# Optimization experiments

Hardware: AMD Instinct MI355X
Metric: run time of the kernel (lower is better)

## Reference

```python
import jax, jax.numpy as jnp
import numpy as np

K = 3          # deform conv kernel size
PAD = 1        # (K-1)//2
DG = 4         # deformable groups
C_IN = 256     # sum(in_channel_list)
C_OUT = 256


def setup_inputs() -> dict:
    key = jax.random.key(0)
    k0, k1, k2, k3, k4, k5 = jax.random.split(key, 6)
    B, H, W = 2, 64, 256
    x0 = jax.random.normal(k0, (B, 64, H, W), dtype=jnp.float32)
    x1 = jax.random.normal(k1, (B, 64, H, W), dtype=jnp.float32)
    x2 = jax.random.normal(k2, (B, 128, H, W), dtype=jnp.float32)
    # conv_offset: 1x1 conv, weight zero-inited in the module; we use small
    # random weights so offsets are spatially varying (nontrivial sampling).
    w_off = jax.random.normal(k3, (DG * K * K * 2, C_IN), dtype=jnp.float32) * 0.01
    b_off = jax.random.normal(k4, (DG * K * K * 2,), dtype=jnp.float32) * 0.5
    # deform conv weight [O, C, K*K] (flat kernel, row-major i*K+j), no bias (mmcv DeformConv)
    w_def = jax.random.normal(k5, (C_OUT, C_IN, K * K), dtype=jnp.float32) / np.sqrt(C_IN * K * K)
    return {"x0": x0, "x1": x1, "x2": x2, "w_off": w_off, "b_off": b_off, "w_def": w_def}


def _deform_gather(xg, py, px):
    # xg: [B, DG, Cg, H, W] grouped input; py/px: [B, DG, K2, H, W] abs sample coords
    B, dg, Cg, H, W = xg.shape
    K2 = py.shape[2]
    y0f = jnp.floor(py)
    x0f = jnp.floor(px)
    wy = py - y0f  # fractional parts
    wx = px - x0f
    y0 = y0f.astype(jnp.int32)
    x0 = x0f.astype(jnp.int32)
    xf = xg.reshape(B, dg, Cg, H * W)

    def corner(yi, xi, w):
        valid = ((yi >= 0) & (yi <= H - 1) & (xi >= 0) & (xi <= W - 1)).astype(xg.dtype)
        idx = jnp.clip(yi, 0, H - 1) * W + jnp.clip(xi, 0, W - 1)   # [B,dg,K2,H,W]
        idxf = idx.reshape(B, dg, 1, K2 * H * W)
        g = jnp.take_along_axis(xf, jnp.broadcast_to(idxf, (B, dg, Cg, K2 * H * W)), axis=-1)
        g = g.reshape(B, dg, Cg, K2, H, W)
        return g * (w * valid)[:, :, None]  # broadcast over Cg

    return (corner(y0, x0, (1.0 - wy) * (1.0 - wx))
            + corner(y0, x0 + 1, (1.0 - wy) * wx)
            + corner(y0 + 1, x0, wy * (1.0 - wx))
            + corner(y0 + 1, x0 + 1, wy * wx))  # [B,dg,Cg,K2,H,W]


def reference(x0, x1, x2, w_off, b_off, w_def):
    x = jnp.concatenate([x0, x1, x2], axis=1)  # [B, C, H, W]
    B, C, H, W = x.shape
    # 1x1 offset conv
    off = jnp.einsum('bchw,oc->bohw', x, w_off) + b_off[None, :, None, None]
    off = off.reshape(B, DG, K * K, 2, H, W)
    dy = off[:, :, :, 0]  # [B,DG,K2,H,W]
    dx = off[:, :, :, 1]
    ky, kx = jnp.meshgrid(jnp.arange(K), jnp.arange(K), indexing='ij')
    ky = ky.reshape(-1).astype(jnp.float32)
    kx = kx.reshape(-1).astype(jnp.float32)
    hh = jnp.arange(H, dtype=jnp.float32)
    ww = jnp.arange(W, dtype=jnp.float32)
    py = hh[None, None, None, :, None] - PAD + ky[None, None, :, None, None] + dy
    px = ww[None, None, None, None, :] - PAD + kx[None, None, :, None, None] + dx
    xg = x.reshape(B, DG, C // DG, H, W)
    samp = _deform_gather(xg, py, px).reshape(B, C, K * K, H, W)
    out = jnp.einsum('bckhw,ock->bohw', samp, w_def)
    return jax.nn.relu(out)
```

## Files before the change

kernel.cpp:

```cpp
#include <hip/hip_runtime.h>


constexpr int H_ = 64, W_ = 256;
constexpr int HWsz = H_ * W_;
constexpr int OC_ = 256;
constexpr int WMAIN_ELEMS = 72 * 16 * 64 * 8;
constexpr int WOFFB_ELEMS = 8 * 5 * 64 * 8;
constexpr size_t XT_ELEMS = (size_t)8 * HWsz * 64;

using f32x4 = __attribute__((ext_vector_type(4))) float;
using s16x8 = __attribute__((ext_vector_type(8))) short;
using u16x8 = __attribute__((ext_vector_type(8))) unsigned short;
using u16x4 = __attribute__((ext_vector_type(4))) unsigned short;

__device__ __forceinline__ unsigned short f2bf(float f) {
    unsigned u = __float_as_uint(f);
    return (unsigned short)((u + 0x7fffu + ((u >> 16) & 1u)) >> 16);
}
__device__ __forceinline__ float bf2f(unsigned short u) {
    return __uint_as_float((unsigned)u << 16);
}
__device__ __forceinline__ void gload_lds16(const void* g, void* l) {
    __builtin_amdgcn_global_load_lds(
        (const __attribute__((address_space(1))) void*)g,
        (__attribute__((address_space(3))) void*)l, 16, 0, 0);
}


__global__ __launch_bounds__(256) void wprep_kernel(const float* __restrict__ w_def,
                                                    const float* __restrict__ w_off,
                                                    unsigned short* __restrict__ w2) {
    int i = blockIdx.x * 256 + threadIdx.x;
    if (i < WMAIN_ELEMS) {
        int j = i & 7, lane = (i >> 3) & 63, t = (i >> 9) & 15, gkh = i >> 13;
        int half = gkh & 1, gk = gkh >> 1;
        int k = gk % 9, g = gk / 9;
        int oc = t * 16 + (lane & 15);
        int cin = g * 64 + half * 32 + (lane >> 4) * 8 + j;
        w2[i] = f2bf(w_def[(size_t)oc * 2304 + (size_t)cin * 9 + k]);
    } else if (i < WMAIN_ELEMS + WOFFB_ELEMS) {
        int i2 = i - WMAIN_ELEMS;
        int j = i2 & 7, lane = (i2 >> 3) & 63, idx = i2 >> 9;
        int t = idx % 5, c8 = idx / 5;
        int o = t * 16 + (lane & 15);
        int ch = c8 * 32 + (lane >> 4) * 8 + j;
        float v = (o < 72) ? w_off[o * 256 + ch] : 0.f;
        w2[i] = f2bf(v);
    }
}

__global__ __launch_bounds__(256) void xprep_kernel(const float* __restrict__ x0,
                                                    const float* __restrict__ x1,
                                                    const float* __restrict__ x2,
                                                    unsigned short* __restrict__ xt) {
    __shared__ unsigned short tl[256][66];
    const int bg = blockIdx.x >> 6;
    const int y  = blockIdx.x & 63;
    const int b  = bg >> 2, g = bg & 3;
    const int tid = threadIdx.x;
    const float* src = (g == 0) ? x0 + (size_t)b * 64 * HWsz
                     : (g == 1) ? x1 + (size_t)b * 64 * HWsz
                     : x2 + (size_t)b * 128 * HWsz + (size_t)(g - 2) * 64 * HWsz;
    src += y * W_;
    for (int c = 0; c < 64; ++c)
        tl[tid][c] = f2bf(src[(size_t)c * HWsz + tid]);
    __syncthreads();
    unsigned short* dst = xt + ((size_t)bg * HWsz + y * W_) * 64;
    #pragma unroll
    for (int s = 0; s < 8; ++s) {
        int si = s * 256 + tid;
        int px = si >> 3, q = si & 7;
        u16x8 v;
        #pragma unroll
        for (int j = 0; j < 8; ++j) v[j] = tl[px][q * 8 + j];
        *(u16x8*)(dst + (size_t)px * 64 + q * 8) = v;
    }
}


struct GPre {
    float w00, w01, w10, w11;
    u16x4 c00, c01, c10, c11;
};

__global__ __launch_bounds__(512, 4) void deform64_kernel(
    const unsigned short* __restrict__ xt, const float* __restrict__ b_off,
    const unsigned short* __restrict__ w2, float* __restrict__ out)
{
    __shared__ float off_lds[72 * 64];
    __shared__ __align__(16) unsigned short Bbuf[2][8192];
    __shared__ __align__(16) unsigned short sbuf[2][2560];

    const int tid  = threadIdx.x;
    const int lane = tid & 63;
    const int wv   = tid >> 6;
    const int bid  = ((blockIdx.x & 7) << 6) | (blockIdx.x >> 3);
    const int xt4  = bid & 3;
    const int h    = (bid >> 2) & 63;
    const int b    = bid >> 8;
    const int xbase = xt4 * 64;
    const int nh   = wv & 1;
    const int pg   = wv >> 1;
    const int p16  = lane & 15;
    const int cq   = lane >> 4;
    const int bp   = wv * 8 + (lane >> 3);
    const int chg  = lane & 7;

    const unsigned short* xtb = xt + (size_t)b * 4 * HWsz * 64;

    if (wv < 4) {
        f32x4 oa[5];
        #pragma unroll
        for (int t = 0; t < 5; ++t) {
            int o = t * 16 + p16;
            float bv = (o < 72) ? b_off[o] : 0.f;
            oa[t][0] = bv; oa[t][1] = bv; oa[t][2] = bv; oa[t][3] = bv;
        }
        const int pixg = h * W_ + xbase + wv * 16;
        #pragma unroll
        for (int c8 = 0; c8 < 8; ++c8) {
            const unsigned short* ap = xtb + (size_t)(c8 >> 1) * HWsz * 64
                                     + (size_t)(pixg + p16) * 64 + (c8 & 1) * 32 + cq * 8;
            s16x8 a = *(const s16x8*)ap;
            const unsigned short* wb = w2 + WMAIN_ELEMS + (size_t)(c8 * 5) * 512;
            #pragma unroll
            for (int t = 0; t < 5; ++t) {
                s16x8 bf = *(const s16x8*)(wb + t * 512 + lane * 8);
                oa[t] = __builtin_amdgcn_mfma_f32_16x16x32_bf16(a, bf, oa[t], 0, 0, 0);
            }
        }
        #pragma unroll
        for (int t = 0; t < 5; ++t) {
            int o = t * 16 + p16;
            if (o < 72) {
                #pragma unroll
                for (int r = 0; r < 4; ++r)
                    off_lds[o * 64 + wv * 16 + cq * 4 + r] = oa[t][r];
            }
        }
    }
    __syncthreads();

    auto stageB = [&](int gkh, int bsel) {
        const char* src = (const char*)w2 + (size_t)gkh * 16384 + (size_t)tid * 16;
        char* dst = (char*)&Bbuf[bsel][0] + wv * 1024;
        gload_lds16(src, dst);
        gload_lds16(src + 8192, dst + 8192);
    };
    auto gpre = [&](int gkh) -> GPre {
        const int half = gkh & 1, gk = gkh >> 1;
        const int k = gk % 9, g = gk / 9;
        const int ky = k / 3, kx = k % 3;
        float dy = off_lds[(2 * gk) * 64 + bp];
        float dx = off_lds[(2 * gk + 1) * 64 + bp];
        float fy = (float)(h - 1 + ky) + dy;
        float fx = (float)(xbase + bp - 1 + kx) + dx;
        float y0f = floorf(fy), x0f = floorf(fx);
        float wy = fy - y0f, wx = fx - x0f;
        int iy0 = (int)y0f, ix0 = (int)x0f;
        int iy1 = iy0 + 1, ix1 = ix0 + 1;
        float vy0 = (iy0 >= 0 && iy0 < H_) ? 1.f : 0.f;
        float vy1 = (iy1 >= 0 && iy1 < H_) ? 1.f : 0.f;
        float vx0 = (ix0 >= 0 && ix0 < W_) ? 1.f : 0.f;
        float vx1 = (ix1 >= 0 && ix1 < W_) ? 1.f : 0.f;
        GPre G;
        G.w00 = (1.f - wy) * (1.f - wx) * vy0 * vx0;
        G.w01 = (1.f - wy) * wx * vy0 * vx1;
        G.w10 = wy * (1.f - wx) * vy1 * vx0;
        G.w11 = wy * wx * vy1 * vx1;
        int cy0 = min(max(iy0, 0), H_ - 1), cy1 = min(max(iy1, 0), H_ - 1);
        int cx0 = min(max(ix0, 0), W_ - 1), cx1 = min(max(ix1, 0), W_ - 1);
        const int eb = half * 32 + chg * 4;
        const unsigned short* src = xtb + (size_t)g * HWsz * 64;
        G.c00 = *(const u16x4*)(src + (cy0 * W_ + cx0) * 64 + eb);
        G.c01 = *(const u16x4*)(src + (cy0 * W_ + cx1) * 64 + eb);
        G.c10 = *(const u16x4*)(src + (cy1 * W_ + cx0) * 64 + eb);
        G.c11 = *(const u16x4*)(src + (cy1 * W_ + cx1) * 64 + eb);
        return G;
    };
    auto gpost = [&](const GPre& G, int bsel) {
        u16x4 res;
        #pragma unroll
        for (int j = 0; j < 4; ++j) {
            float v = fmaf(G.w00, bf2f(G.c00[j]), fmaf(G.w01, bf2f(G.c01[j]),
                      fmaf(G.w10, bf2f(G.c10[j]), G.w11 * bf2f(G.c11[j]))));
            res[j] = f2bf(v);
        }
        *(u16x4*)&sbuf[bsel][bp * 40 + chg * 4] = res;
    };

    f32x4 acc[8];
    #pragma unroll
    for (int t = 0; t < 8; ++t) { acc[t][0]=0; acc[t][1]=0; acc[t][2]=0; acc[t][3]=0; }

    stageB(0, 0);
    {
        GPre G0 = gpre(0);
        gpost(G0, 0);
    }
    __syncthreads();

    const int arow = (pg * 16 + p16) * 40 + cq * 8;
    const unsigned short* bbase0 = &Bbuf[0][0] + (nh * 8) * 512 + lane * 8;
    const unsigned short* bbase1 = &Bbuf[1][0] + (nh * 8) * 512 + lane * 8;

    for (int i = 0; i < 72; ++i) {
        const int cur = i & 1;
        GPre G;
        const bool pf = (i < 71);
        if (pf) {
            stageB(i + 1, cur ^ 1);
            G = gpre(i + 1);
        }
        __builtin_amdgcn_sched_barrier(0);
        s16x8 a = *(const s16x8*)&sbuf[cur][arow];
        const unsigned short* bb = cur ? bbase1 : bbase0;
        #pragma unroll
        for (int t = 0; t < 8; ++t) {
            s16x8 bf = *(const s16x8*)(bb + t * 512);
            acc[t] = __builtin_amdgcn_mfma_f32_16x16x32_bf16(a, bf, acc[t], 0, 0, 0);
        }
        __builtin_amdgcn_sched_barrier(0);
        if (pf) gpost(G, cur ^ 1);
        __syncthreads();
    }

    const size_t obase = (size_t)b * OC_ * HWsz + (size_t)h * W_
                       + xbase + pg * 16 + cq * 4;
    #pragma unroll
    for (int t = 0; t < 8; ++t) {
        int oc = nh * 128 + t * 16 + p16;
        float4 r;
        r.x = fmaxf(acc[t][0], 0.f);
        r.y = fmaxf(acc[t][1], 0.f);
        r.z = fmaxf(acc[t][2], 0.f);
        r.w = fmaxf(acc[t][3], 0.f);
        *(float4*)(out + obase + (size_t)oc * HWsz) = r;
    }
}


struct Geom {
    float w00, w01, w10, w11;
    int o00, o01, o10, o11;
    const float* base;
};

__device__ __forceinline__ Geom make_geom(
    int gkh, const float* offp, int h, int wbase, int p, int cq,
    const float* xA, const float* xB, const float* xC)
{
    const int half = gkh & 1, gk = gkh >> 1;
    const int k = gk % 9, g = gk / 9;
    const int ky = k / 3, kx = k % 3;
    float dy = offp[(2 * gk) * 16 + p];
    float dx = offp[(2 * gk + 1) * 16 + p];
    float fy = (float)(h - 1 + ky) + dy;
    float fx = (float)(wbase + p - 1 + kx) + dx;
    float y0f = floorf(fy), x0f = floorf(fx);
    float wy = fy - y0f, wx = fx - x0f;
    int iy0 = (int)y0f, ix0 = (int)x0f;
    int iy1 = iy0 + 1, ix1 = ix0 + 1;
    float vy0 = (iy0 >= 0 && iy0 < H_) ? 1.f : 0.f;
    float vy1 = (iy1 >= 0 && iy1 < H_) ? 1.f : 0.f;
    float vx0 = (ix0 >= 0 && ix0 < W_) ? 1.f : 0.f;
    float vx1 = (ix1 >= 0 && ix1 < W_) ? 1.f : 0.f;
    Geom gm;
    gm.w00 = (1.f - wy) * (1.f - wx) * vy0 * vx0;
    gm.w01 = (1.f - wy) * wx * vy0 * vx1;
    gm.w10 = wy * (1.f - wx) * vy1 * vx0;
    gm.w11 = wy * wx * vy1 * vx1;
    int cy0 = min(max(iy0, 0), H_ - 1), cy1 = min(max(iy1, 0), H_ - 1);
    int cx0 = min(max(ix0, 0), W_ - 1), cx1 = min(max(ix1, 0), W_ - 1);
    int choff = (half * 32 + cq * 8) * HWsz;
    gm.o00 = choff + cy0 * W_ + cx0;
    gm.o01 = choff + cy0 * W_ + cx1;
    gm.o10 = choff + cy1 * W_ + cx0;
    gm.o11 = choff + cy1 * W_ + cx1;
    gm.base = (g == 0) ? xA : (g == 1) ? xB : (g == 2) ? xC : xC + (size_t)64 * HWsz;
    return gm;
}

#define GATHER(J, Cv) do { \
    Cv.x = gm.base[gm.o00 + (J) * HWsz]; \
    Cv.y = gm.base[gm.o01 + (J) * HWsz]; \
    Cv.z = gm.base[gm.o10 + (J) * HWsz]; \
    Cv.w = gm.base[gm.o11 + (J) * HWsz]; \
} while (0)

#define COMB(Cv, IDX) \
    a[IDX] = (short)f2bf(fmaf(w00c, Cv.x, fmaf(w01c, Cv.y, fmaf(w10c, Cv.z, w11c * Cv.w))))

template<bool USE_WS>
__global__ __launch_bounds__(128, 3) void deform_kernel(
    const float* __restrict__ x0, const float* __restrict__ x1,
    const float* __restrict__ x2,
    const float* __restrict__ w_off, const float* __restrict__ b_off,
    const float* __restrict__ w_def, const unsigned short* __restrict__ w2,
    float* __restrict__ out)
{
    __shared__ float off_lds[2][72 * 16];

    const int tid  = threadIdx.x;
    const int lane = tid & 63;
    const int wv   = tid >> 6;
    const int bid  = ((blockIdx.x & 7) << 8) | (blockIdx.x >> 3);
    const int nh   = wv;
    const int ws_  = bid & 15;
    const int h    = (bid >> 4) & 63;
    const int b    = bid >> 10;
    const int p    = lane & 15;
    const int cq   = lane >> 4;
    const int wbase = ws_ * 16;
    const int pix  = h * W_ + wbase;

    const float* xA = x0 + (size_t)b * 64  * HWsz;
    const float* xB = x1 + (size_t)b * 64  * HWsz;
    const float* xC = x2 + (size_t)b * 128 * HWsz;

    f32x4 oa[5];
    #pragma unroll
    for (int t = 0; t < 5; ++t) {
        int o = t * 16 + p;
        float bv = (o < 72) ? b_off[o] : 0.f;
        oa[t][0] = bv; oa[t][1] = bv; oa[t][2] = bv; oa[t][3] = bv;
    }
    #pragma unroll
    for (int c8 = 0; c8 < 8; ++c8) {
        const float* src = (c8 < 2) ? xA + (size_t)c8 * 32 * HWsz
                         : (c8 < 4) ? xB + (size_t)(c8 - 2) * 32 * HWsz
                                    : xC + (size_t)(c8 - 4) * 32 * HWsz;
        s16x8 a;
        #pragma unroll
        for (int j = 0; j < 8; ++j)
            a[j] = (short)f2bf(src[(cq * 8 + j) * HWsz + pix + p]);
        #pragma unroll
        for (int t = 0; t < 5; ++t) {
            int o = t * 16 + p;
            s16x8 bf;
            if (USE_WS) {
                bf = *(const s16x8*)(w2 + WMAIN_ELEMS + (size_t)(c8 * 5 + t) * 512 + lane * 8);
            } else {
                #pragma unroll
                for (int j = 0; j < 8; ++j)
                    bf[j] = (o < 72) ? (short)f2bf(w_off[o * 256 + c8 * 32 + cq * 8 + j])
                                     : (short)0;
            }
            oa[t] = __builtin_amdgcn_mfma_f32_16x16x32_bf16(a, bf, oa[t], 0, 0, 0);
        }
    }
    #pragma unroll
    for (int t = 0; t < 5; ++t) {
        int o = t * 16 + p;
        if (o < 72) {
            #pragma unroll
            for (int r = 0; r < 4; ++r)
                off_lds[wv][o * 16 + cq * 4 + r] = oa[t][r];
        }
    }

    f32x4 acc0={0,0,0,0},acc1={0,0,0,0},acc2={0,0,0,0},acc3={0,0,0,0};
    f32x4 acc4={0,0,0,0},acc5={0,0,0,0},acc6={0,0,0,0},acc7={0,0,0,0};
    const float* offp = &off_lds[wv][0];

    for (int gkh = 0; gkh < 72; ++gkh) {
        Geom gm = make_geom(gkh, offp, h, wbase, p, cq, xA, xB, xC);
        float4 c0, c1, c2, c3, c4, c5, c6, c7;
        GATHER(0, c0); GATHER(1, c1); GATHER(2, c2); GATHER(3, c3);
        GATHER(4, c4); GATHER(5, c5); GATHER(6, c6); GATHER(7, c7);
        float w00c = gm.w00, w01c = gm.w01, w10c = gm.w10, w11c = gm.w11;
        s16x8 a;
        COMB(c0, 0); COMB(c1, 1); COMB(c2, 2); COMB(c3, 3);
        COMB(c4, 4); COMB(c5, 5); COMB(c6, 6); COMB(c7, 7);
        const int half = gkh & 1, gk = gkh >> 1;
        const int k = gk % 9, g = gk / 9;
        const int cbase = g * 64 + half * 32 + cq * 8;
        f32x4* accp[8] = {&acc0,&acc1,&acc2,&acc3,&acc4,&acc5,&acc6,&acc7};
        #pragma unroll
        for (int t = 0; t < 8; ++t) {
            int oc = nh * 128 + t * 16 + p;
            s16x8 bf;
            if (USE_WS) {
                bf = *(const s16x8*)(w2 + gkh * 8192 + nh * 4096 + t * 512 + lane * 8);
            } else {
                #pragma unroll
                for (int j = 0; j < 8; ++j)
                    bf[j] = (short)f2bf(w_def[(size_t)oc * 2304 + (size_t)(cbase + j) * 9 + k]);
            }
            *accp[t] = __builtin_amdgcn_mfma_f32_16x16x32_bf16(a, bf, *accp[t], 0, 0, 0);
        }
    }

    const size_t obase = (size_t)b * OC_ * HWsz + (size_t)h * W_ + wbase + cq * 4;
    f32x4 accs[8] = {acc0, acc1, acc2, acc3, acc4, acc5, acc6, acc7};
    #pragma unroll
    for (int t = 0; t < 8; ++t) {
        int oc = nh * 128 + t * 16 + p;
        float4 r;
        r.x = fmaxf(accs[t][0], 0.f);
        r.y = fmaxf(accs[t][1], 0.f);
        r.z = fmaxf(accs[t][2], 0.f);
        r.w = fmaxf(accs[t][3], 0.f);
        *(float4*)(out + obase + (size_t)oc * HWsz) = r;
    }
}

extern "C" void kernel_launch(void* const* d_in, const int* in_sizes, int n_in,
                              void* d_out, int out_size, void* d_ws, size_t ws_size,
                              hipStream_t stream) {
    const float* x0    = (const float*)d_in[0];
    const float* x1    = (const float*)d_in[1];
    const float* x2    = (const float*)d_in[2];
    const float* w_off = (const float*)d_in[3];
    const float* b_off = (const float*)d_in[4];
    const float* w_def = (const float*)d_in[5];
    float* out = (float*)d_out;

    const size_t w2_bytes   = (size_t)(WMAIN_ELEMS + WOFFB_ELEMS) * 2;
    const size_t full_bytes = (XT_ELEMS + WMAIN_ELEMS + WOFFB_ELEMS) * 2;

    if (ws_size >= full_bytes) {
        unsigned short* xt = (unsigned short*)d_ws;
        unsigned short* w2 = xt + XT_ELEMS;
        hipLaunchKernelGGL(xprep_kernel, dim3(512), dim3(256), 0, stream, x0, x1, x2, xt);
        hipLaunchKernelGGL(wprep_kernel, dim3((WMAIN_ELEMS + WOFFB_ELEMS) / 256), dim3(256),
                           0, stream, w_def, w_off, w2);
        hipLaunchKernelGGL(deform64_kernel, dim3(512), dim3(512), 0, stream,
                           xt, b_off, w2, out);
    } else if (ws_size >= w2_bytes) {
        unsigned short* w2 = (unsigned short*)d_ws;
        hipLaunchKernelGGL(wprep_kernel, dim3((WMAIN_ELEMS + WOFFB_ELEMS) / 256), dim3(256),
                           0, stream, w_def, w_off, w2);
        hipLaunchKernelGGL((deform_kernel<true>), dim3(2048), dim3(128), 0, stream,
                           x0, x1, x2, w_off, b_off, w_def, w2, out);
    } else {
        hipLaunchKernelGGL((deform_kernel<false>), dim3(2048), dim3(128), 0, stream,
                           x0, x1, x2, w_off, b_off, w_def, (const unsigned short*)nullptr, out);
    }
}
```

Measured before the change: 113.2 us.

## Process full 64-channel group per iteration with 16-byte gathers and swizzled LDS

The main loop now handles a whole (group, tap) with 64 channels per iteration instead of two 32-channel halves, halving the number of iterations and barriers. Each lane gathers 8 bf16 channels per corner with 16-byte loads and converts pairs with the packed bf16 convert instruction, writing an XOR-swizzled sample tile to LDS. B weights are single-buffered and staged after the second barrier, while the gather for step i+2 is issued one iteration ahead. The aim is fewer barriers and wider loads, at the cost of more registers held for gather data and less overlap of the weight loads, which are no longer double-buffered.

```diff
diff --git a/kernel.cpp b/kernel.cpp
--- a/kernel.cpp
+++ b/kernel.cpp
@@ -11,7 +11,6 @@
 using f32x4 = __attribute__((ext_vector_type(4))) float;
 using s16x8 = __attribute__((ext_vector_type(8))) short;
 using u16x8 = __attribute__((ext_vector_type(8))) unsigned short;
-using u16x4 = __attribute__((ext_vector_type(4))) unsigned short;
 
 __device__ __forceinline__ unsigned short f2bf(float f) {
     unsigned u = __float_as_uint(f);
@@ -19,6 +18,11 @@
 }
 __device__ __forceinline__ float bf2f(unsigned short u) {
     return __uint_as_float((unsigned)u << 16);
+}
+__device__ __forceinline__ unsigned cvt_pk_bf16(float lo, float hi) {
+    unsigned r;
+    asm("v_cvt_pk_bf16_f32 %0, %1, %2" : "=v"(r) : "v"(lo), "v"(hi));
+    return r;
 }
 __device__ __forceinline__ void gload_lds16(const void* g, void* l) {
     __builtin_amdgcn_global_load_lds(
@@ -80,7 +84,7 @@
 
 struct GPre {
     float w00, w01, w10, w11;
-    u16x4 c00, c01, c10, c11;
+    u16x8 c00, c01, c10, c11;
 };
 
 __global__ __launch_bounds__(512, 4) void deform64_kernel(
@@ -88,8 +92,8 @@
     const unsigned short* __restrict__ w2, float* __restrict__ out)
 {
     __shared__ float off_lds[72 * 64];
-    __shared__ __align__(16) unsigned short Bbuf[2][8192];
-    __shared__ __align__(16) unsigned short sbuf[2][2560];
+    __shared__ __align__(16) unsigned short Bbuf[16384];
+    __shared__ __align__(16) unsigned short sbuf16[8192];
 
     const int tid  = threadIdx.x;
     const int lane = tid & 63;
@@ -105,6 +109,12 @@
     const int cq   = lane >> 4;
     const int bp   = wv * 8 + (lane >> 3);
     const int chg  = lane & 7;
+    const int halfw = chg >> 2;
+    const int cqw   = chg & 3;
+    const int slotw = ((cqw << 4) | (bp & 15)) ^ cqw ^ (halfw << 2);
+    const int sbw   = halfw * 2048 + (bp >> 4) * 512 + slotw * 8;
+    const int roff0 = pg * 512 + (lane ^ cq) * 8;
+    const int roff1 = 2048 + pg * 512 + (lane ^ cq ^ 4) * 8;
 
     const unsigned short* xtb = xt + (size_t)b * 4 * HWsz * 64;
 
@@ -141,14 +151,14 @@
     }
     __syncthreads();
 
-    auto stageB = [&](int gkh, int bsel) {
-        const char* src = (const char*)w2 + (size_t)gkh * 16384 + (size_t)tid * 16;
-        char* dst = (char*)&Bbuf[bsel][0] + wv * 1024;
-        gload_lds16(src, dst);
-        gload_lds16(src + 8192, dst + 8192);
+    auto stageB = [&](int gk) {
+        const char* src = (const char*)w2 + (size_t)gk * 32768 + (size_t)tid * 16;
+        char* dst = (char*)&Bbuf[0] + wv * 1024;
+        #pragma unroll
+        for (int q = 0; q < 4; ++q)
+            gload_lds16(src + q * 8192, dst + q * 8192);
     };
-    auto gpre = [&](int gkh) -> GPre {
-        const int half = gkh & 1, gk = gkh >> 1;
+    auto gpre = [&](int gk) -> GPre {
         const int k = gk % 9, g = gk / 9;
         const int ky = k / 3, kx = k % 3;
         float dy = off_lds[(2 * gk) * 64 + bp];
@@ -170,59 +180,64 @@
         G.w11 = wy * wx * vy1 * vx1;
         int cy0 = min(max(iy0, 0), H_ - 1), cy1 = min(max(iy1, 0), H_ - 1);
         int cx0 = min(max(ix0, 0), W_ - 1), cx1 = min(max(ix1, 0), W_ - 1);
-        const int eb = half * 32 + chg * 4;
-        const unsigned short* src = xtb + (size_t)g * HWsz * 64;
-        G.c00 = *(const u16x4*)(src + (cy0 * W_ + cx0) * 64 + eb);
-        G.c01 = *(const u16x4*)(src + (cy0 * W_ + cx1) * 64 + eb);
-        G.c10 = *(const u16x4*)(src + (cy1 * W_ + cx0) * 64 + eb);
-        G.c11 = *(const u16x4*)(src + (cy1 * W_ + cx1) * 64 + eb);
+        const unsigned short* src = xtb + (size_t)g * HWsz * 64 + chg * 8;
+        G.c00 = *(const u16x8*)(src + (cy0 * W_ + cx0) * 64);
+        G.c01 = *(const u16x8*)(src + (cy0 * W_ + cx1) * 64);
+        G.c10 = *(const u16x8*)(src + (cy1 * W_ + cx0) * 64);
+        G.c11 = *(const u16x8*)(src + (cy1 * W_ + cx1) * 64);
         return G;
     };
-    auto gpost = [&](const GPre& G, int bsel) {
-        u16x4 res;
-        #pragma unroll
-        for (int j = 0; j < 4; ++j) {
-            float v = fmaf(G.w00, bf2f(G.c00[j]), fmaf(G.w01, bf2f(G.c01[j]),
-                      fmaf(G.w10, bf2f(G.c10[j]), G.w11 * bf2f(G.c11[j]))));
-            res[j] = f2bf(v);
-        }
-        *(u16x4*)&sbuf[bsel][bp * 40 + chg * 4] = res;
+    auto gpost = [&](const GPre& G, int buf) {
+        unsigned d[4];
+        #pragma unroll
+        for (int q = 0; q < 4; ++q) {
+            float v0 = fmaf(G.w00, bf2f(G.c00[2*q]), fmaf(G.w01, bf2f(G.c01[2*q]),
+                       fmaf(G.w10, bf2f(G.c10[2*q]), G.w11 * bf2f(G.c11[2*q]))));
+            float v1 = fmaf(G.w00, bf2f(G.c00[2*q+1]), fmaf(G.w01, bf2f(G.c01[2*q+1]),
+                       fmaf(G.w10, bf2f(G.c10[2*q+1]), G.w11 * bf2f(G.c11[2*q+1]))));
+            d[q] = cvt_pk_bf16(v0, v1);
+        }
+        uint4 v4; v4.x = d[0]; v4.y = d[1]; v4.z = d[2]; v4.w = d[3];
+        *(uint4*)&sbuf16[buf * 4096 + sbw] = v4;
     };
 
     f32x4 acc[8];
     #pragma unroll
     for (int t = 0; t < 8; ++t) { acc[t][0]=0; acc[t][1]=0; acc[t][2]=0; acc[t][3]=0; }
 
-    stageB(0, 0);
+    stageB(0);
     {
         GPre G0 = gpre(0);
         gpost(G0, 0);
     }
-    __syncthreads();
-
-    const int arow = (pg * 16 + p16) * 40 + cq * 8;
-    const unsigned short* bbase0 = &Bbuf[0][0] + (nh * 8) * 512 + lane * 8;
-    const unsigned short* bbase1 = &Bbuf[1][0] + (nh * 8) * 512 + lane * 8;
-
-    for (int i = 0; i < 72; ++i) {
+    GPre G = gpre(1);
+
+    for (int i = 0; i < 36; ++i) {
+        __syncthreads();
         const int cur = i & 1;
-        GPre G;
-        const bool pf = (i < 71);
-        if (pf) {
-            stageB(i + 1, cur ^ 1);
-            G = gpre(i + 1);
-        }
-        __builtin_amdgcn_sched_barrier(0);
-        s16x8 a = *(const s16x8*)&sbuf[cur][arow];
-        const unsigned short* bb = cur ? bbase1 : bbase0;
-        #pragma unroll
-        for (int t = 0; t < 8; ++t) {
-            s16x8 bf = *(const s16x8*)(bb + t * 512);
-            acc[t] = __builtin_amdgcn_mfma_f32_16x16x32_bf16(a, bf, acc[t], 0, 0, 0);
-        }
-        __builtin_amdgcn_sched_barrier(0);
-        if (pf) gpost(G, cur ^ 1);
+        const unsigned short* sb = sbuf16 + cur * 4096;
+        {
+            s16x8 a = *(const s16x8*)(sb + roff0);
+            const unsigned short* bb = Bbuf + nh * 4096 + lane * 8;
+            #pragma unroll
+            for (int t = 0; t < 8; ++t) {
+                s16x8 bf = *(const s16x8*)(bb + t * 512);
+                acc[t] = __builtin_amdgcn_mfma_f32_16x16x32_bf16(a, bf, acc[t], 0, 0, 0);
+            }
+        }
+        {
+            s16x8 a = *(const s16x8*)(sb + roff1);
+            const unsigned short* bb = Bbuf + 8192 + nh * 4096 + lane * 8;
+            #pragma unroll
+            for (int t = 0; t < 8; ++t) {
+                s16x8 bf = *(const s16x8*)(bb + t * 512);
+                acc[t] = __builtin_amdgcn_mfma_f32_16x16x32_bf16(a, bf, acc[t], 0, 0, 0);
+            }
+        }
+        if (i < 35) gpost(G, cur ^ 1);
         __syncthreads();
+        if (i < 35) stageB(i + 1);
+        if (i < 34) G = gpre(i + 2);
     }
 
     const size_t obase = (size_t)b * OC_ * HWsz + (size_t)h * W_
```

New measurement: 91.09 us. 1.24x faster.
